# Kernel tuning notes

Hardware: AMD Instinct MI355X
Metric: run time of the kernel (lower is better)

The kernel has to match this reference:

```python
import jax, jax.numpy as jnp
from jax import lax
import numpy as np

B, N, H, K = 64, 256, 1024, 3  # batch, num_proposals, hidden_dim, conv kernel size
LN_EPS = 1e-5


def setup_inputs() -> dict:
    key = jax.random.key(0)
    k1, k2, k3 = jax.random.split(key, 3)
    scale = 1.0 / np.sqrt(H)
    return {
        "f": jax.random.normal(k1, (B, N, H), dtype=jnp.float32),
        "k": jax.random.normal(k2, (B, N, H), dtype=jnp.float32),
        "W_lin": jax.random.normal(k3, (N * K, H), dtype=jnp.float32) * scale,
        "b_lin": jnp.zeros((N * K,), dtype=jnp.float32),
        "ln_gamma": jnp.ones((H,), dtype=jnp.float32),
        "ln_beta": jnp.zeros((H,), dtype=jnp.float32),
    }


def _conv_one(x, w):
    # x: [N, H] (channels, length); w: [N_out, N_in, K]
    # PyTorch F.conv1d is cross-correlation, same as lax conv with no flip.
    y = lax.conv_general_dilated(
        x[None], w, window_strides=(1,), padding="SAME",
        dimension_numbers=("NCH", "OIH", "NCH"))
    return y[0]  # [N, H]


def reference(f, k, W_lin, b_lin, ln_gamma, ln_beta):
    # Dynamic weight generation: [B, N, H] -> [B, N, N*K] -> [B, N, N, K]
    weight = jnp.einsum("bnh,oh->bno", f, W_lin) + b_lin
    weight = weight.reshape(B, N, N, K)
    # Per-sample dynamic conv1d over the hidden dim (batched via vmap)
    out = jax.vmap(_conv_one)(k, weight)  # [B, N, H]
    # LayerNorm over hidden dim
    mu = jnp.mean(out, axis=-1, keepdims=True)
    var = jnp.var(out, axis=-1, keepdims=True)
    out = (out - mu) * lax.rsqrt(var + LN_EPS) * ln_gamma + ln_beta
    return out
```

## Files before the change

### kernel.cpp

```cpp
#include <hip/hip_runtime.h>
#include <math.h>

#define Bsz 64
#define Nn  256
#define Hh  1024
#define NK  768

typedef __bf16 bf16;
typedef bf16 bf16x4 __attribute__((ext_vector_type(4)));
typedef bf16 bf16x8 __attribute__((ext_vector_type(8)));
typedef float floatx4 __attribute__((ext_vector_type(4)));

#define KT_ROWS   1026
#define KT_BSTRIDE (KT_ROWS * 256)

__device__ __forceinline__ void gl_lds16(const bf16* g, bf16* l) {
    __builtin_amdgcn_global_load_lds(
        (__attribute__((address_space(1))) void*)(g),
        (__attribute__((address_space(3))) void*)(l), 16, 0, 0);
}

__global__ __launch_bounds__(256) void cast2_kernel(
    const float* __restrict__ f, const float* __restrict__ wl,
    bf16* __restrict__ fbf, bf16* __restrict__ wlbf)
{
    int i = blockIdx.x * 256 + threadIdx.x;
    if (i < 4194304) {
        float4 v = ((const float4*)f)[i];
        bf16x4 o = { (bf16)v.x, (bf16)v.y, (bf16)v.z, (bf16)v.w };
        ((bf16x4*)fbf)[i] = o;
    } else {
        int j = i - 4194304;
        if (j < 196608) {
            float4 v = ((const float4*)wl)[j];
            bf16x4 o = { (bf16)v.x, (bf16)v.y, (bf16)v.z, (bf16)v.w };
            ((bf16x4*)wlbf)[j] = o;
        }
    }
}

__global__ __launch_bounds__(256) void kT_kernel(
    const float* __restrict__ kin, bf16* __restrict__ kTp)
{
    __shared__ bf16 T[64 * 72];
    const int tid = threadIdx.x;
    const int b = blockIdx.z, i0 = blockIdx.y * 64, h0 = blockIdx.x * 64;
    const float* src = kin + ((size_t)b << 18);
    bf16* dstb = kTp + (size_t)b * KT_BSTRIDE;

    if (blockIdx.x == 0 && blockIdx.y == 0) {
        dstb[tid] = (bf16)0.f;
        dstb[(size_t)1025 * 256 + tid] = (bf16)0.f;
    }
    #pragma unroll
    for (int j = 0; j < 4; ++j) {
        int s = tid + j * 256;
        int il = s >> 4, c4 = s & 15;
        float4 v = *(const float4*)&src[(size_t)(i0 + il) * Hh + h0 + c4 * 4];
        T[(c4 * 4 + 0) * 72 + il] = (bf16)v.x;
        T[(c4 * 4 + 1) * 72 + il] = (bf16)v.y;
        T[(c4 * 4 + 2) * 72 + il] = (bf16)v.z;
        T[(c4 * 4 + 3) * 72 + il] = (bf16)v.w;
    }
    __syncthreads();
    #pragma unroll
    for (int p = 0; p < 2; ++p) {
        int hl = (tid >> 3) + p * 32;
        int q  = tid & 7;
        bf16x8 v = *(const bf16x8*)&T[hl * 72 + q * 8];
        *(bf16x8*)&dstb[(size_t)(h0 + hl + 1) * 256 + i0 + q * 8] = v;
    }
}

__global__ __launch_bounds__(256) void gemm1_mfma(
    const bf16* __restrict__ A,
    const bf16* __restrict__ Bw,
    const float* __restrict__ bias,
    bf16* __restrict__ wgt3)
{
    __shared__ bf16 smem[14336];
    bf16* As = smem;
    bf16* Bs = smem + 8192;
    const int tid  = threadIdx.x;
    const int wave = tid >> 6, lane = tid & 63;
    const int row0 = blockIdx.y * 128;
    const int col0 = blockIdx.x * 96;

    const bf16* gA[4]; bf16* lA[4];
    #pragma unroll
    for (int j = 0; j < 4; ++j) {
        int s = tid + j * 256;
        int reg = s >> 9, rem = s & 511, row = rem >> 2, quad = rem & 3;
        gA[j] = A + (size_t)(row0 + row) * Hh + reg * 32 + quad * 8;
        lA[j] = As + s * 8;
    }
    const bf16* gB[3]; bf16* lB[3];
    #pragma unroll
    for (int j = 0; j < 3; ++j) {
        int s = tid + j * 256;
        int reg = s / 384, rem = s - reg * 384, row = rem >> 2, quad = rem & 3;
        gB[j] = Bw + (size_t)(col0 + row) * Hh + reg * 32 + quad * 8;
        lB[j] = Bs + s * 8;
    }

    const int wm = wave & 1, wn = wave >> 1;
    const int fm = lane & 15, koct = (lane >> 4) * 8;

    floatx4 zero = {0.f, 0.f, 0.f, 0.f};
    floatx4 acc[4][3];
    #pragma unroll
    for (int i = 0; i < 4; ++i)
        #pragma unroll
        for (int j = 0; j < 3; ++j) acc[i][j] = zero;

    for (int k0 = 0; k0 < Hh; k0 += 64) {
        #pragma unroll
        for (int j = 0; j < 4; ++j) gl_lds16(gA[j] + k0, lA[j]);
        #pragma unroll
        for (int j = 0; j < 3; ++j) gl_lds16(gB[j] + k0, lB[j]);
        __syncthreads();
        #pragma unroll
        for (int q = 0; q < 2; ++q) {
            bf16x8 af[4], bfr[3];
            #pragma unroll
            for (int mt = 0; mt < 4; ++mt)
                af[mt] = *(const bf16x8*)&As[q * 4096 + (wm * 64 + mt * 16 + fm) * 32 + koct];
            #pragma unroll
            for (int nt = 0; nt < 3; ++nt)
                bfr[nt] = *(const bf16x8*)&Bs[q * 3072 + (wn * 48 + nt * 16 + fm) * 32 + koct];
            #pragma unroll
            for (int mt = 0; mt < 4; ++mt)
                #pragma unroll
                for (int nt = 0; nt < 3; ++nt)
                    acc[mt][nt] = __builtin_amdgcn_mfma_f32_16x16x32_bf16(
                        af[mt], bfr[nt], acc[mt][nt], 0, 0, 0);
        }
        __syncthreads();
    }

    const int b  = row0 >> 8;
    const int nb = row0 & 255;
    bf16* Cs = smem;
    #pragma unroll
    for (int nt = 0; nt < 3; ++nt) {
        int c = wn * 48 + nt * 16 + fm;
        float bl = bias[col0 + c];
        #pragma unroll
        for (int mt = 0; mt < 4; ++mt) {
            int rb = wm * 64 + mt * 16 + (lane >> 4) * 4;
            #pragma unroll
            for (int r = 0; r < 4; ++r)
                Cs[(rb + r) * 104 + c] = (bf16)(acc[mt][nt][r] + bl);
        }
    }
    __syncthreads();
    const int i0 = blockIdx.x * 32;
    #pragma unroll
    for (int j = 0; j < 6; ++j) {
        int s = tid + j * 256;
        int t = s / 512, rem = s & 511, n = rem >> 2, q8 = rem & 3;
        bf16x8 v;
        #pragma unroll
        for (int u = 0; u < 8; ++u)
            v[u] = Cs[n * 104 + (q8 * 8 + u) * 3 + t];
        *(bf16x8*)&wgt3[((size_t)(b * 3 + t) << 16) + ((size_t)(nb + n) << 8) + i0 + q8 * 8] = v;
    }
}

__global__ __launch_bounds__(256, 2) void conv_mfma(
    const bf16* __restrict__ kTp,
    const bf16* __restrict__ wgt3,
    float* __restrict__ out)
{
    __shared__ bf16 As[12288];
    __shared__ bf16 Ks[8704];
    const int tid  = threadIdx.x;
    const int wave = tid >> 6, lane = tid & 63;
    const int b  = blockIdx.z;
    const int o0 = blockIdx.y * 128;
    const int h0 = blockIdx.x * 256;
    const int wm = wave & 1, wn = wave >> 1;
    const int fm = lane & 15, koct = (lane >> 4) * 8;

    const bf16* gA[6]; bf16* lA[6];
    #pragma unroll
    for (int j = 0; j < 6; ++j) {
        int s = tid + j * 256;
        int t = s / 512, rem = s & 511, o = rem >> 2, iq = rem & 3;
        gA[j] = wgt3 + ((size_t)(b * 3 + t) << 16) + ((size_t)(o0 + o) << 8) + iq * 8;
        lA[j] = As + s * 8;
    }
    const bf16* kb = kTp + (size_t)b * KT_BSTRIDE;
    const bf16* gK[4]; bf16* lK[4];
    #pragma unroll
    for (int j = 0; j < 4; ++j) {
        int s = tid + j * 256;
        int r = s >> 2, quad = s & 3;
        gK[j] = kb + (size_t)(h0 + r) * 256 + quad * 8;
        lK[j] = Ks + s * 8;
    }

    floatx4 zero = {0.f, 0.f, 0.f, 0.f};
    floatx4 acc[4][8];
    #pragma unroll
    for (int i = 0; i < 4; ++i)
        #pragma unroll
        for (int j = 0; j < 8; ++j) acc[i][j] = zero;

    for (int ic = 0; ic < 8; ++ic) {
        const int i0 = ic * 32;
        __syncthreads();
        #pragma unroll
        for (int j = 0; j < 6; ++j) gl_lds16(gA[j] + i0, lA[j]);
        #pragma unroll
        for (int j = 0; j < 4; ++j) gl_lds16(gK[j] + i0, lK[j]);
        if (tid < 8) {
            int r = 256 + (tid >> 2), q = tid & 3;
            bf16x8 v = *(const bf16x8*)&kb[(size_t)(h0 + r) * 256 + i0 + q * 8];
            *(bf16x8*)&Ks[r * 32 + q * 8] = v;
        }
        __syncthreads();
        #pragma unroll
        for (int t = 0; t < 3; ++t) {
            bf16x8 af[4], bfr[8];
            #pragma unroll
            for (int mt = 0; mt < 4; ++mt)
                af[mt] = *(const bf16x8*)&As[t * 4096 + (wm * 64 + mt * 16 + fm) * 32 + koct];
            #pragma unroll
            for (int nt = 0; nt < 8; ++nt)
                bfr[nt] = *(const bf16x8*)&Ks[(wn * 128 + nt * 16 + fm + t) * 32 + koct];
            #pragma unroll
            for (int mt = 0; mt < 4; ++mt)
                #pragma unroll
                for (int nt = 0; nt < 8; ++nt)
                    acc[mt][nt] = __builtin_amdgcn_mfma_f32_16x16x32_bf16(
                        af[mt], bfr[nt], acc[mt][nt], 0, 0, 0);
        }
    }

    #pragma unroll
    for (int mt = 0; mt < 4; ++mt) {
        int o = o0 + wm * 64 + mt * 16 + (lane >> 4) * 4;
        #pragma unroll
        for (int nt = 0; nt < 8; ++nt) {
            int h = h0 + wn * 128 + nt * 16 + fm;
            #pragma unroll
            for (int r = 0; r < 4; ++r)
                out[((size_t)(b * 256 + o + r) << 10) + h] = acc[mt][nt][r];
        }
    }
}

__global__ __launch_bounds__(256) void ln_kernel(
    float* __restrict__ io, const float* __restrict__ gamma,
    const float* __restrict__ beta)
{
    const int row = blockIdx.x;
    const int tid = threadIdx.x;
    float* p = io + ((size_t)row << 10);
    float4 v = ((const float4*)p)[tid];
    float x[4] = {v.x, v.y, v.z, v.w};
    float s1 = x[0] + x[1] + x[2] + x[3];
    float s2 = x[0]*x[0] + x[1]*x[1] + x[2]*x[2] + x[3]*x[3];
    #pragma unroll
    for (int m = 1; m < 64; m <<= 1) {
        s1 += __shfl_xor(s1, m, 64);
        s2 += __shfl_xor(s2, m, 64);
    }
    __shared__ float r1[4], r2[4];
    if ((tid & 63) == 0) { r1[tid >> 6] = s1; r2[tid >> 6] = s2; }
    __syncthreads();
    float S1 = r1[0] + r1[1] + r1[2] + r1[3];
    float S2 = r2[0] + r2[1] + r2[2] + r2[3];
    float mu   = S1 * (1.0f / 1024.0f);
    float var  = S2 * (1.0f / 1024.0f) - mu * mu;
    float rstd = rsqrtf(var + 1e-5f);
    float4 g  = ((const float4*)gamma)[tid];
    float4 be = ((const float4*)beta)[tid];
    float4 o;
    o.x = (x[0] - mu) * rstd * g.x + be.x;
    o.y = (x[1] - mu) * rstd * g.y + be.y;
    o.z = (x[2] - mu) * rstd * g.z + be.z;
    o.w = (x[3] - mu) * rstd * g.w + be.w;
    ((float4*)p)[tid] = o;
}

extern "C" void kernel_launch(void* const* d_in, const int* in_sizes, int n_in,
                              void* d_out, int out_size, void* d_ws, size_t ws_size,
                              hipStream_t stream) {
    const float* f     = (const float*)d_in[0];
    const float* kin   = (const float*)d_in[1];
    const float* W_lin = (const float*)d_in[2];
    const float* b_lin = (const float*)d_in[3];
    const float* gamma = (const float*)d_in[4];
    const float* beta  = (const float*)d_in[5];
    float* out = (float*)d_out;

    char* ws = (char*)d_ws;
    bf16* fbf  = (bf16*)(ws);
    bf16* kTp  = (bf16*)(ws);
    bf16* wlbf = (bf16*)(ws + 33619968);
    bf16* wgt3 = (bf16*)(ws + 35192832);

    cast2_kernel<<<17152, 256, 0, stream>>>(f, W_lin, fbf, wlbf);
    gemm1_mfma<<<dim3(8, 128), 256, 0, stream>>>(fbf, wlbf, b_lin, wgt3);
    kT_kernel<<<dim3(16, 4, 64), 256, 0, stream>>>(kin, kTp);
    conv_mfma<<<dim3(4, 2, 64), 256, 0, stream>>>(kTp, wgt3, out);
    ln_kernel<<<16384, 256, 0, stream>>>(out, gamma, beta);
}
```

Baseline: 287.0 us.

## Fuse fp32 casts into GEMM loads, merge transpose kernel, shrink conv tile

The separate cast kernel is removed. The weight-generation GEMM now loads fp32 f and W_lin directly and converts them to bf16 in registers before storing to LDS, which avoids writing and re-reading bf16 copies through HBM. The k-transpose work is folded into the same launch as extra blocks, cutting launch count and letting the transpose run alongside the GEMM. The conv kernel's output-row tile drops from 128 to 64 with 3 blocks per CU, giving more blocks and higher occupancy. In exchange the GEMM gives up the asynchronous global-to-LDS path for synchronous register loads, and the fp32 input data it reads is twice as large.

```diff
diff --git a/kernel.cpp b/kernel.cpp
--- a/kernel.cpp
+++ b/kernel.cpp
@@ -20,86 +20,77 @@
         (__attribute__((address_space(3))) void*)(l), 16, 0, 0);
 }
 
-__global__ __launch_bounds__(256) void cast2_kernel(
-    const float* __restrict__ f, const float* __restrict__ wl,
-    bf16* __restrict__ fbf, bf16* __restrict__ wlbf)
-{
-    int i = blockIdx.x * 256 + threadIdx.x;
-    if (i < 4194304) {
-        float4 v = ((const float4*)f)[i];
-        bf16x4 o = { (bf16)v.x, (bf16)v.y, (bf16)v.z, (bf16)v.w };
-        ((bf16x4*)fbf)[i] = o;
-    } else {
-        int j = i - 4194304;
-        if (j < 196608) {
-            float4 v = ((const float4*)wl)[j];
-            bf16x4 o = { (bf16)v.x, (bf16)v.y, (bf16)v.z, (bf16)v.w };
-            ((bf16x4*)wlbf)[j] = o;
-        }
-    }
-}
-
-__global__ __launch_bounds__(256) void kT_kernel(
-    const float* __restrict__ kin, bf16* __restrict__ kTp)
-{
-    __shared__ bf16 T[64 * 72];
-    const int tid = threadIdx.x;
-    const int b = blockIdx.z, i0 = blockIdx.y * 64, h0 = blockIdx.x * 64;
-    const float* src = kin + ((size_t)b << 18);
-    bf16* dstb = kTp + (size_t)b * KT_BSTRIDE;
-
-    if (blockIdx.x == 0 && blockIdx.y == 0) {
-        dstb[tid] = (bf16)0.f;
-        dstb[(size_t)1025 * 256 + tid] = (bf16)0.f;
-    }
-    #pragma unroll
-    for (int j = 0; j < 4; ++j) {
-        int s = tid + j * 256;
-        int il = s >> 4, c4 = s & 15;
-        float4 v = *(const float4*)&src[(size_t)(i0 + il) * Hh + h0 + c4 * 4];
-        T[(c4 * 4 + 0) * 72 + il] = (bf16)v.x;
-        T[(c4 * 4 + 1) * 72 + il] = (bf16)v.y;
-        T[(c4 * 4 + 2) * 72 + il] = (bf16)v.z;
-        T[(c4 * 4 + 3) * 72 + il] = (bf16)v.w;
-    }
-    __syncthreads();
-    #pragma unroll
-    for (int p = 0; p < 2; ++p) {
-        int hl = (tid >> 3) + p * 32;
-        int q  = tid & 7;
-        bf16x8 v = *(const bf16x8*)&T[hl * 72 + q * 8];
-        *(bf16x8*)&dstb[(size_t)(h0 + hl + 1) * 256 + i0 + q * 8] = v;
-    }
-}
-
-__global__ __launch_bounds__(256) void gemm1_mfma(
-    const bf16* __restrict__ A,
-    const bf16* __restrict__ Bw,
+__device__ __forceinline__ bf16x8 cvt8(float4 a, float4 b) {
+    bf16x8 v;
+    v[0] = (bf16)a.x; v[1] = (bf16)a.y; v[2] = (bf16)a.z; v[3] = (bf16)a.w;
+    v[4] = (bf16)b.x; v[5] = (bf16)b.y; v[6] = (bf16)b.z; v[7] = (bf16)b.w;
+    return v;
+}
+
+__global__ __launch_bounds__(256) void prep_gemm_kernel(
+    const float* __restrict__ A32,
+    const float* __restrict__ W32,
     const float* __restrict__ bias,
-    bf16* __restrict__ wgt3)
+    const float* __restrict__ kin,
+    bf16* __restrict__ wgt3,
+    bf16* __restrict__ kTp)
 {
     __shared__ bf16 smem[14336];
+    const int tid = threadIdx.x;
+
+    if (blockIdx.x >= 1024) {
+        int id = blockIdx.x - 1024;
+        int hb = id & 15, ib = (id >> 4) & 3, b = id >> 6;
+        int i0 = ib * 64, h0 = hb * 64;
+        const float* src = kin + ((size_t)b << 18);
+        bf16* dstb = kTp + (size_t)b * KT_BSTRIDE;
+        bf16* T = smem;
+
+        if (hb == 0 && ib == 0) {
+            dstb[tid] = (bf16)0.f;
+            dstb[(size_t)1025 * 256 + tid] = (bf16)0.f;
+        }
+        #pragma unroll
+        for (int j = 0; j < 4; ++j) {
+            int s = tid + j * 256;
+            int il = s >> 4, c4 = s & 15;
+            float4 v = *(const float4*)&src[(size_t)(i0 + il) * Hh + h0 + c4 * 4];
+            T[(c4 * 4 + 0) * 72 + il] = (bf16)v.x;
+            T[(c4 * 4 + 1) * 72 + il] = (bf16)v.y;
+            T[(c4 * 4 + 2) * 72 + il] = (bf16)v.z;
+            T[(c4 * 4 + 3) * 72 + il] = (bf16)v.w;
+        }
+        __syncthreads();
+        #pragma unroll
+        for (int p = 0; p < 2; ++p) {
+            int hl = (tid >> 3) + p * 32;
+            int q  = tid & 7;
+            bf16x8 v = *(const bf16x8*)&T[hl * 72 + q * 8];
+            *(bf16x8*)&dstb[(size_t)(h0 + hl + 1) * 256 + i0 + q * 8] = v;
+        }
+        return;
+    }
+
     bf16* As = smem;
     bf16* Bs = smem + 8192;
-    const int tid  = threadIdx.x;
     const int wave = tid >> 6, lane = tid & 63;
-    const int row0 = blockIdx.y * 128;
-    const int col0 = blockIdx.x * 96;
-
-    const bf16* gA[4]; bf16* lA[4];
+    const int row0 = (blockIdx.x >> 3) * 128;
+    const int col0 = (blockIdx.x & 7) * 96;
+
+    const float* gA[4]; bf16* lA[4];
     #pragma unroll
     for (int j = 0; j < 4; ++j) {
         int s = tid + j * 256;
         int reg = s >> 9, rem = s & 511, row = rem >> 2, quad = rem & 3;
-        gA[j] = A + (size_t)(row0 + row) * Hh + reg * 32 + quad * 8;
+        gA[j] = A32 + (size_t)(row0 + row) * Hh + reg * 32 + quad * 8;
         lA[j] = As + s * 8;
     }
-    const bf16* gB[3]; bf16* lB[3];
+    const float* gB[3]; bf16* lB[3];
     #pragma unroll
     for (int j = 0; j < 3; ++j) {
         int s = tid + j * 256;
         int reg = s / 384, rem = s - reg * 384, row = rem >> 2, quad = rem & 3;
-        gB[j] = Bw + (size_t)(col0 + row) * Hh + reg * 32 + quad * 8;
+        gB[j] = W32 + (size_t)(col0 + row) * Hh + reg * 32 + quad * 8;
         lB[j] = Bs + s * 8;
     }
 
@@ -114,10 +105,22 @@
         for (int j = 0; j < 3; ++j) acc[i][j] = zero;
 
     for (int k0 = 0; k0 < Hh; k0 += 64) {
-        #pragma unroll
-        for (int j = 0; j < 4; ++j) gl_lds16(gA[j] + k0, lA[j]);
-        #pragma unroll
-        for (int j = 0; j < 3; ++j) gl_lds16(gB[j] + k0, lB[j]);
+        float4 av[4][2], bv[3][2];
+        #pragma unroll
+        for (int j = 0; j < 4; ++j) {
+            av[j][0] = ((const float4*)(gA[j] + k0))[0];
+            av[j][1] = ((const float4*)(gA[j] + k0))[1];
+        }
+        #pragma unroll
+        for (int j = 0; j < 3; ++j) {
+            bv[j][0] = ((const float4*)(gB[j] + k0))[0];
+            bv[j][1] = ((const float4*)(gB[j] + k0))[1];
+        }
+        __syncthreads();
+        #pragma unroll
+        for (int j = 0; j < 4; ++j) *(bf16x8*)lA[j] = cvt8(av[j][0], av[j][1]);
+        #pragma unroll
+        for (int j = 0; j < 3; ++j) *(bf16x8*)lB[j] = cvt8(bv[j][0], bv[j][1]);
         __syncthreads();
         #pragma unroll
         for (int q = 0; q < 2; ++q) {
@@ -135,8 +138,8 @@
                     acc[mt][nt] = __builtin_amdgcn_mfma_f32_16x16x32_bf16(
                         af[mt], bfr[nt], acc[mt][nt], 0, 0, 0);
         }
-        __syncthreads();
-    }
+    }
+    __syncthreads();
 
     const int b  = row0 >> 8;
     const int nb = row0 & 255;
@@ -154,7 +157,7 @@
         }
     }
     __syncthreads();
-    const int i0 = blockIdx.x * 32;
+    const int i0 = (blockIdx.x & 7) * 32;
     #pragma unroll
     for (int j = 0; j < 6; ++j) {
         int s = tid + j * 256;
@@ -167,26 +170,26 @@
     }
 }
 
-__global__ __launch_bounds__(256, 2) void conv_mfma(
+__global__ __launch_bounds__(256, 3) void conv_mfma(
     const bf16* __restrict__ kTp,
     const bf16* __restrict__ wgt3,
     float* __restrict__ out)
 {
-    __shared__ bf16 As[12288];
-    __shared__ bf16 Ks[8704];
+    __shared__ bf16 As[6144];
+    __shared__ bf16 Ks[8256];
     const int tid  = threadIdx.x;
     const int wave = tid >> 6, lane = tid & 63;
     const int b  = blockIdx.z;
-    const int o0 = blockIdx.y * 128;
+    const int o0 = blockIdx.y * 64;
     const int h0 = blockIdx.x * 256;
     const int wm = wave & 1, wn = wave >> 1;
     const int fm = lane & 15, koct = (lane >> 4) * 8;
 
-    const bf16* gA[6]; bf16* lA[6];
-    #pragma unroll
-    for (int j = 0; j < 6; ++j) {
-        int s = tid + j * 256;
-        int t = s / 512, rem = s & 511, o = rem >> 2, iq = rem & 3;
+    const bf16* gA[3]; bf16* lA[3];
+    #pragma unroll
+    for (int j = 0; j < 3; ++j) {
+        int s = tid + j * 256;
+        int t = s >> 8, rem = s & 255, o = rem >> 2, iq = rem & 3;
         gA[j] = wgt3 + ((size_t)(b * 3 + t) << 16) + ((size_t)(o0 + o) << 8) + iq * 8;
         lA[j] = As + s * 8;
     }
@@ -201,9 +204,9 @@
     }
 
     floatx4 zero = {0.f, 0.f, 0.f, 0.f};
-    floatx4 acc[4][8];
-    #pragma unroll
-    for (int i = 0; i < 4; ++i)
+    floatx4 acc[2][8];
+    #pragma unroll
+    for (int i = 0; i < 2; ++i)
         #pragma unroll
         for (int j = 0; j < 8; ++j) acc[i][j] = zero;
 
@@ -211,7 +214,7 @@
         const int i0 = ic * 32;
         __syncthreads();
         #pragma unroll
-        for (int j = 0; j < 6; ++j) gl_lds16(gA[j] + i0, lA[j]);
+        for (int j = 0; j < 3; ++j) gl_lds16(gA[j] + i0, lA[j]);
         #pragma unroll
         for (int j = 0; j < 4; ++j) gl_lds16(gK[j] + i0, lK[j]);
         if (tid < 8) {
@@ -222,15 +225,15 @@
         __syncthreads();
         #pragma unroll
         for (int t = 0; t < 3; ++t) {
-            bf16x8 af[4], bfr[8];
-            #pragma unroll
-            for (int mt = 0; mt < 4; ++mt)
-                af[mt] = *(const bf16x8*)&As[t * 4096 + (wm * 64 + mt * 16 + fm) * 32 + koct];
+            bf16x8 af[2], bfr[8];
+            #pragma unroll
+            for (int mt = 0; mt < 2; ++mt)
+                af[mt] = *(const bf16x8*)&As[t * 2048 + (wm * 32 + mt * 16 + fm) * 32 + koct];
             #pragma unroll
             for (int nt = 0; nt < 8; ++nt)
                 bfr[nt] = *(const bf16x8*)&Ks[(wn * 128 + nt * 16 + fm + t) * 32 + koct];
             #pragma unroll
-            for (int mt = 0; mt < 4; ++mt)
+            for (int mt = 0; mt < 2; ++mt)
                 #pragma unroll
                 for (int nt = 0; nt < 8; ++nt)
                     acc[mt][nt] = __builtin_amdgcn_mfma_f32_16x16x32_bf16(
@@ -239,8 +242,8 @@
     }
 
     #pragma unroll
-    for (int mt = 0; mt < 4; ++mt) {
-        int o = o0 + wm * 64 + mt * 16 + (lane >> 4) * 4;
+    for (int mt = 0; mt < 2; ++mt) {
+        int o = o0 + wm * 32 + mt * 16 + (lane >> 4) * 4;
         #pragma unroll
         for (int nt = 0; nt < 8; ++nt) {
             int h = h0 + wn * 128 + nt * 16 + fm;
@@ -297,14 +300,10 @@
     float* out = (float*)d_out;
 
     char* ws = (char*)d_ws;
-    bf16* fbf  = (bf16*)(ws);
     bf16* kTp  = (bf16*)(ws);
-    bf16* wlbf = (bf16*)(ws + 33619968);
-    bf16* wgt3 = (bf16*)(ws + 35192832);
-
-    cast2_kernel<<<17152, 256, 0, stream>>>(f, W_lin, fbf, wlbf);
-    gemm1_mfma<<<dim3(8, 128), 256, 0, stream>>>(fbf, wlbf, b_lin, wgt3);
-    kT_kernel<<<dim3(16, 4, 64), 256, 0, stream>>>(kin, kTp);
-    conv_mfma<<<dim3(4, 2, 64), 256, 0, stream>>>(kTp, wgt3, out);
+    bf16* wgt3 = (bf16*)(ws + 33619968);
+
+    prep_gemm_kernel<<<5120, 256, 0, stream>>>(f, W_lin, b_lin, kin, wgt3, kTp);
+    conv_mfma<<<dim3(4, 4, 64), 256, 0, stream>>>(kTp, wgt3, out);
     ln_kernel<<<16384, 256, 0, stream>>>(out, gamma, beta);
 }
```

Result: slower. 300.6 us (+4.7%).
